# Performance work log

Measured on AMD Instinct MI355X. Metric: run time of the kernel, lower is better.

Reference implementation:

```python
import jax, jax.numpy as jnp
import numpy as np


def setup_inputs() -> dict:
    key = jax.random.key(0)
    k1, k2 = jax.random.split(key)
    bs, dim = 8192, 768
    nl_vec = jax.random.normal(k1, (bs, dim), dtype=jnp.float32)
    code_vec = jax.random.normal(k2, (bs, dim), dtype=jnp.float32)
    return {"nl_vec": nl_vec, "code_vec": code_vec}


def reference(nl_vec, code_vec):
    # scores[i, j] = <nl_vec[i], code_vec[j]>  (GEMM form of the broadcast mult-sum)
    scores = jnp.einsum("id,jd->ij", nl_vec, code_vec)  # [bs, bs]
    bs = scores.shape[0]
    # CrossEntropyLoss with labels = arange(bs): mean over rows of (logsumexp - diag)
    lse = jax.nn.logsumexp(scores, axis=-1)             # [bs]
    diag = jnp.einsum("id,id->i", nl_vec, code_vec)     # scores[i, i]
    loss = jnp.mean(lse - diag)
    return (loss, code_vec, nl_vec)
```

## Files before the change

### kernel.cpp

```cpp
#include <hip/hip_runtime.h>

#define BS     8192
#define DIM    768
#define NPART  32
#define BM     256
#define BN     256
#define BK     64
#define NKT    (DIM / BK)
#define L1B    128
#define L1R    (BS / L1B)

typedef __bf16 bfrag_t __attribute__((ext_vector_type(8)));
typedef float  facc_t  __attribute__((ext_vector_type(4)));

typedef const __attribute__((address_space(1))) void gv_t;
typedef __attribute__((address_space(3))) void lv_t;

__device__ __forceinline__ void gll16(const void* g, void* l) {
  __builtin_amdgcn_global_load_lds((gv_t*)g, (lv_t*)l, 16, 0, 0);
}

__device__ __forceinline__ unsigned short f2bf(float f) {
  union { float f; unsigned u; } v; v.f = f;
  unsigned u = v.u;
  return (unsigned short)((u + 0x7FFFu + ((u >> 16) & 1u)) >> 16);
}

__global__ void prep_kernel(const float* __restrict__ nl, const float* __restrict__ cd,
                            float* __restrict__ cd_copy, float* __restrict__ nl_copy,
                            unsigned short* __restrict__ nlb, unsigned short* __restrict__ cdb,
                            float* __restrict__ dg) {
  const int lane = threadIdx.x & 63;
  const int wave = threadIdx.x >> 6;
  const int row  = blockIdx.x * 4 + wave;
  const size_t rbase = (size_t)row * DIM;
  const float4* ar = reinterpret_cast<const float4*>(nl + rbase);
  const float4* br = reinterpret_cast<const float4*>(cd + rbase);
  float4* wa = reinterpret_cast<float4*>(nl_copy + rbase);
  float4* wb = reinterpret_cast<float4*>(cd_copy + rbase);
  ushort4* ba = reinterpret_cast<ushort4*>(nlb + rbase);
  ushort4* bb = reinterpret_cast<ushort4*>(cdb + rbase);

  float s = 0.f;
#pragma unroll
  for (int i = 0; i < 3; ++i) {
    int idx = lane + 64 * i;
    float4 x = ar[idx];
    float4 y = br[idx];
    wa[idx] = x;
    wb[idx] = y;
    ushort4 xb, yb;
    xb.x = f2bf(x.x); xb.y = f2bf(x.y); xb.z = f2bf(x.z); xb.w = f2bf(x.w);
    yb.x = f2bf(y.x); yb.y = f2bf(y.y); yb.z = f2bf(y.z); yb.w = f2bf(y.w);
    ba[idx] = xb;
    bb[idx] = yb;
    s += x.x * y.x + x.y * y.y + x.z * y.z + x.w * y.w;
  }
#pragma unroll
  for (int off = 32; off; off >>= 1) s += __shfl_xor(s, off, 64);
  if (lane == 0) dg[row] = s;
}

__global__ __launch_bounds__(512, 2) void gemm_lse_kernel(
    const unsigned short* __restrict__ Abf,
    const unsigned short* __restrict__ Bbf,
    float* __restrict__ pm, float* __restrict__ pl) {
  __shared__ __align__(16) unsigned short As[2 * BM * BK];
  __shared__ __align__(16) unsigned short Bs[2 * BN * BK];

  const int tid  = threadIdx.x;
  const int lane = tid & 63;
  const int wave = tid >> 6;
  const int wm   = wave >> 2;
  const int wn   = wave & 3;
  const int l15  = lane & 15;
  const int l4   = lane >> 4;
  const int swz  = l15 & 7;
  const int cb   = blockIdx.x;
  const int rb   = blockIdx.y;

  const int k8x0 = ((0 * 4 + l4) ^ swz) * 8;
  const int k8x1 = ((1 * 4 + l4) ^ swz) * 8;

  size_t aoff[4], boff[4];
  int ldso[4];
#pragma unroll
  for (int p = 0; p < 4; ++p) {
    int u   = p * 512 + tid;
    int row = u >> 3;
    int c8  = (u & 7) ^ (row & 7);
    aoff[p] = (size_t)(rb * BM + row) * DIM + c8 * 8;
    boff[p] = (size_t)(cb * BN + row) * DIM + c8 * 8;
    ldso[p] = u * 8;
  }

#define STG_A(kt, h) do { \
    gll16(Abf + aoff[2*(h)]   + (size_t)(kt) * BK, &As[(((kt) & 1) << 14) + ldso[2*(h)]]); \
    gll16(Abf + aoff[2*(h)+1] + (size_t)(kt) * BK, &As[(((kt) & 1) << 14) + ldso[2*(h)+1]]); \
  } while (0)
#define STG_B(kt, h) do { \
    gll16(Bbf + boff[2*(h)]   + (size_t)(kt) * BK, &Bs[(((kt) & 1) << 14) + ldso[2*(h)]]); \
    gll16(Bbf + boff[2*(h)+1] + (size_t)(kt) * BK, &Bs[(((kt) & 1) << 14) + ldso[2*(h)+1]]); \
  } while (0)

  bfrag_t af[2][2];
  bfrag_t bf[4][2];
  facc_t  acc[8][4];
#pragma unroll
  for (int mt = 0; mt < 8; ++mt)
#pragma unroll
    for (int nt = 0; nt < 4; ++nt) acc[mt][nt] = (facc_t){0.f, 0.f, 0.f, 0.f};

#define DS_A(b, q) do { \
    _Pragma("unroll") \
    for (int i_ = 0; i_ < 2; ++i_) { \
      const unsigned short* pA_ = &As[(b) * 16384 + (wm * 128 + (2*(q)+i_) * 16 + l15) * 64]; \
      af[i_][0] = *reinterpret_cast<const bfrag_t*>(pA_ + k8x0); \
      af[i_][1] = *reinterpret_cast<const bfrag_t*>(pA_ + k8x1); \
    } } while (0)
#define DS_B(b) do { \
    _Pragma("unroll") \
    for (int n_ = 0; n_ < 4; ++n_) { \
      const unsigned short* pB_ = &Bs[(b) * 16384 + (wn * 64 + n_ * 16 + l15) * 64]; \
      bf[n_][0] = *reinterpret_cast<const bfrag_t*>(pB_ + k8x0); \
      bf[n_][1] = *reinterpret_cast<const bfrag_t*>(pB_ + k8x1); \
    } } while (0)
#define MFMA_Q(q) do { \
    _Pragma("unroll") \
    for (int i_ = 0; i_ < 2; ++i_) \
      _Pragma("unroll") \
      for (int n_ = 0; n_ < 4; ++n_) { \
        acc[2*(q)+i_][n_] = __builtin_amdgcn_mfma_f32_16x16x32_bf16(af[i_][0], bf[n_][0], acc[2*(q)+i_][n_], 0, 0, 0); \
        acc[2*(q)+i_][n_] = __builtin_amdgcn_mfma_f32_16x16x32_bf16(af[i_][1], bf[n_][1], acc[2*(q)+i_][n_], 0, 0, 0); \
      } } while (0)

#define PH_TOP() do { __builtin_amdgcn_s_barrier(); \
    asm volatile("s_waitcnt lgkmcnt(0)" ::: "memory"); \
    __builtin_amdgcn_sched_barrier(0); \
    __builtin_amdgcn_s_setprio(1); } while (0)
#define PH_BOT() do { __builtin_amdgcn_s_setprio(0); \
    __builtin_amdgcn_sched_barrier(0); \
    __builtin_amdgcn_s_barrier(); } while (0)
#define PH_BOT_VM(n) do { __builtin_amdgcn_s_setprio(0); \
    __builtin_amdgcn_sched_barrier(0); \
    asm volatile("s_waitcnt vmcnt(" #n ")" ::: "memory"); \
    __builtin_amdgcn_sched_barrier(0); \
    __builtin_amdgcn_s_barrier(); } while (0)

  STG_B(0, 0); STG_B(0, 1); STG_A(0, 0); STG_A(0, 1); STG_B(1, 0); STG_B(1, 1);
  asm volatile("s_waitcnt vmcnt(4)" ::: "memory");
  __builtin_amdgcn_sched_barrier(0);
  __builtin_amdgcn_s_barrier();

  for (int t = 0; t < 5; ++t) {
    const int k0 = 2 * t;
    DS_B(0); DS_A(0, 0); STG_A(k0 + 1, 0); STG_A(k0 + 1, 1);
    PH_TOP(); MFMA_Q(0); PH_BOT();
    DS_A(0, 1); STG_B(k0 + 2, 0);
    PH_TOP(); MFMA_Q(1); PH_BOT();
    DS_A(0, 2); STG_B(k0 + 2, 1);
    PH_TOP(); MFMA_Q(2); PH_BOT();
    DS_A(0, 3);
    PH_TOP(); MFMA_Q(3); PH_BOT_VM(4);
    DS_B(1); DS_A(1, 0); STG_A(k0 + 2, 0);
    PH_TOP(); MFMA_Q(0); PH_BOT();
    DS_A(1, 1); STG_A(k0 + 2, 1);
    PH_TOP(); MFMA_Q(1); PH_BOT();
    DS_A(1, 2); STG_B(k0 + 3, 0);
    PH_TOP(); MFMA_Q(2); PH_BOT();
    DS_A(1, 3); STG_B(k0 + 3, 1);
    PH_TOP(); MFMA_Q(3); PH_BOT_VM(4);
  }

  DS_B(0); DS_A(0, 0); STG_A(11, 0); STG_A(11, 1);
  PH_TOP(); MFMA_Q(0); PH_BOT();
  DS_A(0, 1);
  PH_TOP(); MFMA_Q(1); PH_BOT();
  DS_A(0, 2);
  PH_TOP(); MFMA_Q(2); PH_BOT();
  DS_A(0, 3);
  PH_TOP(); MFMA_Q(3); PH_BOT_VM(0);
  DS_B(1); DS_A(1, 0);
  PH_TOP(); MFMA_Q(0); PH_BOT();
  DS_A(1, 1);
  PH_TOP(); MFMA_Q(1); PH_BOT();
  DS_A(1, 2);
  PH_TOP(); MFMA_Q(2); PH_BOT();
  DS_A(1, 3);
  PH_TOP(); MFMA_Q(3); PH_BOT();

  float* cm = reinterpret_cast<float*>(As);
  float* cl = reinterpret_cast<float*>(Bs);
#pragma unroll
  for (int mt = 0; mt < 8; ++mt)
#pragma unroll
    for (int r = 0; r < 4; ++r) {
      float v0 = acc[mt][0][r], v1 = acc[mt][1][r], v2 = acc[mt][2][r], v3 = acc[mt][3][r];
      float m = fmaxf(fmaxf(v0, v1), fmaxf(v2, v3));
      float l = __expf(v0 - m) + __expf(v1 - m) + __expf(v2 - m) + __expf(v3 - m);
#pragma unroll
      for (int mask = 1; mask < 16; mask <<= 1) {
        float om = __shfl_xor(m, mask, 64);
        float ol = __shfl_xor(l, mask, 64);
        float mn = fmaxf(m, om);
        l = l * __expf(m - mn) + ol * __expf(om - mn);
        m = mn;
      }
      if (l15 == 0) {
        int rl = wm * 128 + mt * 16 + l4 * 4 + r;
        cm[wn * BM + rl] = m;
        cl[wn * BM + rl] = l;
      }
    }
  __syncthreads();
  if (tid < BM) {
    float m0 = cm[tid],          l0 = cl[tid];
    float m1 = cm[BM + tid],     l1 = cl[BM + tid];
    float m2 = cm[2 * BM + tid], l2 = cl[2 * BM + tid];
    float m3 = cm[3 * BM + tid], l3 = cl[3 * BM + tid];
    float mn = fmaxf(fmaxf(m0, m1), fmaxf(m2, m3));
    float ll = l0 * __expf(m0 - mn) + l1 * __expf(m1 - mn) +
               l2 * __expf(m2 - mn) + l3 * __expf(m3 - mn);
    size_t g = (size_t)(rb * BM + tid) * NPART + cb;
    pm[g] = mn;
    pl[g] = ll;
  }

#undef STG_A
#undef STG_B
#undef DS_A
#undef DS_B
#undef MFMA_Q
#undef PH_TOP
#undef PH_BOT
#undef PH_BOT_VM
}

__global__ void loss_stage1_kernel(const float* __restrict__ pm, const float* __restrict__ pl,
                                   const float* __restrict__ dg, float* __restrict__ partial) {
  const int tid = threadIdx.x;
  const int r   = blockIdx.x * L1R + tid;

  const float4* pmr = reinterpret_cast<const float4*>(pm + (size_t)r * NPART);
  const float4* plr = reinterpret_cast<const float4*>(pl + (size_t)r * NPART);

  float m = -1e30f, l = 0.f;
#pragma unroll
  for (int q = 0; q < NPART / 4; ++q) {
    float4 mv = pmr[q];
    float4 lv = plr[q];
#pragma unroll
    for (int k = 0; k < 4; ++k) {
      float m2 = (&mv.x)[k], l2 = (&lv.x)[k];
      float mn = fmaxf(m, m2);
      l = l * __expf(m - mn) + l2 * __expf(m2 - mn);
      m = mn;
    }
  }
  float local = m + __logf(l) - dg[r];

#pragma unroll
  for (int off = 32; off; off >>= 1) local += __shfl_xor(local, off, 64);
  if (tid == 0) partial[blockIdx.x] = local;
}

__global__ void loss_stage2_kernel(const float* __restrict__ partial, float* __restrict__ out) {
  const int tid = threadIdx.x;
  float v = partial[tid];
#pragma unroll
  for (int off = 32; off; off >>= 1) v += __shfl_xor(v, off, 64);
  __shared__ float red[2];
  if ((tid & 63) == 0) red[tid >> 6] = v;
  __syncthreads();
  if (tid == 0) out[0] = (red[0] + red[1]) / (float)BS;
}

extern "C" void kernel_launch(void* const* d_in, const int* in_sizes, int n_in,
                              void* d_out, int out_size, void* d_ws, size_t ws_size,
                              hipStream_t stream) {
  const float* nl = (const float*)d_in[0];
  const float* cd = (const float*)d_in[1];
  float* out = (float*)d_out;

  const size_t NEL = (size_t)BS * DIM;

  unsigned short* nlb = (unsigned short*)d_ws;
  unsigned short* cdb = nlb + NEL;
  float* pm = (float*)(cdb + NEL);
  float* pl = pm + (size_t)BS * NPART;
  float* dg = pl + (size_t)BS * NPART;
  float* partial = dg + BS;

  prep_kernel<<<BS / 4, 256, 0, stream>>>(nl, cd, out + 1, out + 1 + NEL, nlb, cdb, dg);
  gemm_lse_kernel<<<dim3(NPART, BS / BM), 512, 0, stream>>>(nlb, cdb, pm, pl);
  loss_stage1_kernel<<<L1B, 64, 0, stream>>>(pm, pl, dg, partial);
  loss_stage2_kernel<<<1, 128, 0, stream>>>(partial, out);
}
```

Before: 251.5 us.

## Rework GEMM main loop to triple-buffered BK=32 pipeline with inline-asm LDS reads

```diff
diff --git a/kernel.cpp b/kernel.cpp
--- a/kernel.cpp
+++ b/kernel.cpp
@@ -5,13 +5,14 @@
 #define NPART  32
 #define BM     256
 #define BN     256
-#define BK     64
+#define BK     32
 #define NKT    (DIM / BK)
 #define L1B    128
 #define L1R    (BS / L1B)
 
 typedef __bf16 bfrag_t __attribute__((ext_vector_type(8)));
 typedef float  facc_t  __attribute__((ext_vector_type(4)));
+typedef float  f4raw   __attribute__((ext_vector_type(4)));
 
 typedef const __attribute__((address_space(1))) void gv_t;
 typedef __attribute__((address_space(3))) void lv_t;
@@ -65,8 +66,7 @@
     const unsigned short* __restrict__ Abf,
     const unsigned short* __restrict__ Bbf,
     float* __restrict__ pm, float* __restrict__ pl) {
-  __shared__ __align__(16) unsigned short As[2 * BM * BK];
-  __shared__ __align__(16) unsigned short Bs[2 * BN * BK];
+  __shared__ __align__(16) unsigned short LDSU[49152];
 
   const int tid  = threadIdx.x;
   const int lane = tid & 63;
@@ -75,122 +75,104 @@
   const int wn   = wave & 3;
   const int l15  = lane & 15;
   const int l4   = lane >> 4;
-  const int swz  = l15 & 7;
-  const int cb   = blockIdx.x;
-  const int rb   = blockIdx.y;
-
-  const int k8x0 = ((0 * 4 + l4) ^ swz) * 8;
-  const int k8x1 = ((1 * 4 + l4) ^ swz) * 8;
-
-  size_t aoff[4], boff[4];
-  int ldso[4];
-#pragma unroll
-  for (int p = 0; p < 4; ++p) {
-    int u   = p * 512 + tid;
-    int row = u >> 3;
-    int c8  = (u & 7) ^ (row & 7);
-    aoff[p] = (size_t)(rb * BM + row) * DIM + c8 * 8;
-    boff[p] = (size_t)(cb * BN + row) * DIM + c8 * 8;
-    ldso[p] = u * 8;
-  }
-
-#define STG_A(kt, h) do { \
-    gll16(Abf + aoff[2*(h)]   + (size_t)(kt) * BK, &As[(((kt) & 1) << 14) + ldso[2*(h)]]); \
-    gll16(Abf + aoff[2*(h)+1] + (size_t)(kt) * BK, &As[(((kt) & 1) << 14) + ldso[2*(h)+1]]); \
-  } while (0)
-#define STG_B(kt, h) do { \
-    gll16(Bbf + boff[2*(h)]   + (size_t)(kt) * BK, &Bs[(((kt) & 1) << 14) + ldso[2*(h)]]); \
-    gll16(Bbf + boff[2*(h)+1] + (size_t)(kt) * BK, &Bs[(((kt) & 1) << 14) + ldso[2*(h)+1]]); \
-  } while (0)
-
-  bfrag_t af[2][2];
-  bfrag_t bf[4][2];
-  facc_t  acc[8][4];
+
+  unsigned lin = blockIdx.y * 32 + blockIdx.x;
+  unsigned swz = (lin & 7) * 128 + (lin >> 3);
+  const int cb = swz & 31;
+  const int rb = swz >> 5;
+
+  const int a0_ = tid >> 3, s0_ = tid & 7, l0_ = s0_ ^ (a0_ & 7);
+  const int grow = 2 * a0_ + ((l0_ >> 2) & 1);
+  const int gc8  = l0_ & 3;
+  const unsigned short* srcA0 = Abf + (size_t)(rb * BM + grow) * DIM + gc8 * 8;
+  const unsigned short* srcB0 = Bbf + (size_t)(cb * BN + grow) * DIM + gc8 * 8;
+  char* dstA0 = (char*)LDSU + tid * 16;
+  char* dstB0 = (char*)LDSU + 49152 + tid * 16;
+
+#define STGA(k) do{ gll16(srcA0 + (size_t)(k) * 32,                    dstA0 + ((k) % 3) * 16384); \
+                    gll16(srcA0 + (size_t)128 * DIM + (size_t)(k) * 32, dstA0 + ((k) % 3) * 16384 + 8192);}while(0)
+#define STGB(k) do{ gll16(srcB0 + (size_t)(k) * 32,                    dstB0 + ((k) % 3) * 16384); \
+                    gll16(srcB0 + (size_t)128 * DIM + (size_t)(k) * 32, dstB0 + ((k) % 3) * 16384 + 8192);}while(0)
+
+  const unsigned lds32 = (unsigned)(uintptr_t)(void*)&LDSU[0];
+  const unsigned physA = ((unsigned)(((l15 & 1) << 2) | l4)) ^ (unsigned)((l15 >> 1) & 7);
+  const unsigned abase = lds32 + (unsigned)(wm * 64 + (l15 >> 1)) * 128 + physA * 16;
+  const unsigned bbase = lds32 + 49152u + (unsigned)(wn * 32 + (l15 >> 1)) * 128 + physA * 16;
+
+  f4raw afL[4], afH[4], bfE[4], bfO[4];
+  facc_t acc[8][4];
 #pragma unroll
   for (int mt = 0; mt < 8; ++mt)
 #pragma unroll
     for (int nt = 0; nt < 4; ++nt) acc[mt][nt] = (facc_t){0.f, 0.f, 0.f, 0.f};
 
-#define DS_A(b, q) do { \
+#define DSR(dst, addr, off) \
+  asm volatile("ds_read_b128 %0, %1 offset:%2" : "=v"(dst) : "v"(addr), "n"(off))
+#define RD4(ARR, base, off) do{ \
+    DSR(ARR[0], base, (off) + 0 * 1024); DSR(ARR[1], base, (off) + 1 * 1024); \
+    DSR(ARR[2], base, (off) + 2 * 1024); DSR(ARR[3], base, (off) + 3 * 1024); }while(0)
+
+#define MFMA_PH(AF, BF, half) do{ \
     _Pragma("unroll") \
-    for (int i_ = 0; i_ < 2; ++i_) { \
-      const unsigned short* pA_ = &As[(b) * 16384 + (wm * 128 + (2*(q)+i_) * 16 + l15) * 64]; \
-      af[i_][0] = *reinterpret_cast<const bfrag_t*>(pA_ + k8x0); \
-      af[i_][1] = *reinterpret_cast<const bfrag_t*>(pA_ + k8x1); \
-    } } while (0)
-#define DS_B(b) do { \
-    _Pragma("unroll") \
-    for (int n_ = 0; n_ < 4; ++n_) { \
-      const unsigned short* pB_ = &Bs[(b) * 16384 + (wn * 64 + n_ * 16 + l15) * 64]; \
-      bf[n_][0] = *reinterpret_cast<const bfrag_t*>(pB_ + k8x0); \
-      bf[n_][1] = *reinterpret_cast<const bfrag_t*>(pB_ + k8x1); \
-    } } while (0)
-#define MFMA_Q(q) do { \
-    _Pragma("unroll") \
-    for (int i_ = 0; i_ < 2; ++i_) \
+    for (int m_ = 0; m_ < 4; ++m_) \
       _Pragma("unroll") \
-      for (int n_ = 0; n_ < 4; ++n_) { \
-        acc[2*(q)+i_][n_] = __builtin_amdgcn_mfma_f32_16x16x32_bf16(af[i_][0], bf[n_][0], acc[2*(q)+i_][n_], 0, 0, 0); \
-        acc[2*(q)+i_][n_] = __builtin_amdgcn_mfma_f32_16x16x32_bf16(af[i_][1], bf[n_][1], acc[2*(q)+i_][n_], 0, 0, 0); \
-      } } while (0)
-
-#define PH_TOP() do { __builtin_amdgcn_s_barrier(); \
-    asm volatile("s_waitcnt lgkmcnt(0)" ::: "memory"); \
-    __builtin_amdgcn_sched_barrier(0); \
-    __builtin_amdgcn_s_setprio(1); } while (0)
-#define PH_BOT() do { __builtin_amdgcn_s_setprio(0); \
-    __builtin_amdgcn_sched_barrier(0); \
-    __builtin_amdgcn_s_barrier(); } while (0)
-#define PH_BOT_VM(n) do { __builtin_amdgcn_s_setprio(0); \
-    __builtin_amdgcn_sched_barrier(0); \
-    asm volatile("s_waitcnt vmcnt(" #n ")" ::: "memory"); \
-    __builtin_amdgcn_sched_barrier(0); \
-    __builtin_amdgcn_s_barrier(); } while (0)
-
-  STG_B(0, 0); STG_B(0, 1); STG_A(0, 0); STG_A(0, 1); STG_B(1, 0); STG_B(1, 1);
-  asm volatile("s_waitcnt vmcnt(4)" ::: "memory");
+      for (int n_ = 0; n_ < 4; ++n_) \
+        acc[(half) * 4 + m_][n_] = __builtin_amdgcn_mfma_f32_16x16x32_bf16( \
+            __builtin_bit_cast(bfrag_t, AF[m_]), __builtin_bit_cast(bfrag_t, BF[n_]), \
+            acc[(half) * 4 + m_][n_], 0, 0, 0); \
+  }while(0)
+
+#define TOPN(n) do{ __builtin_amdgcn_sched_barrier(0); __builtin_amdgcn_s_barrier(); \
+    asm volatile("s_waitcnt lgkmcnt(" #n ")"); __builtin_amdgcn_sched_barrier(0); \
+    __builtin_amdgcn_s_setprio(1);}while(0)
+#define BOT() do{ __builtin_amdgcn_s_setprio(0); __builtin_amdgcn_sched_barrier(0); \
+    __builtin_amdgcn_s_barrier();}while(0)
+#define BOTVM(n) do{ __builtin_amdgcn_s_setprio(0); __builtin_amdgcn_sched_barrier(0); \
+    asm volatile("s_waitcnt vmcnt(" #n ")"); __builtin_amdgcn_sched_barrier(0); \
+    __builtin_amdgcn_s_barrier();}while(0)
+
+#define KT(k, BFC, BFN, VMN) do{ \
+     \
+    RD4(afH, abase, ((k) % 3) * 16384 + 4096); \
+    if ((k) <= 21) STGA((k) + 2); \
+    TOPN(4); \
+    MFMA_PH(afL, BFC, 0); \
+    BOTVM(VMN);                                    \
+     \
+    RD4(BFN, bbase, (((k) + 1) % 3) * 16384); \
+    RD4(afL, abase, (((k) + 1) % 3) * 16384); \
+    if ((k) <= 21) STGB((k) + 2); \
+    TOPN(8); \
+    MFMA_PH(afH, BFC, 1); \
+    BOT(); \
+  }while(0)
+
+  STGA(0); STGB(0); STGA(1); STGB(1);
+  __builtin_amdgcn_sched_barrier(0);
+  asm volatile("s_waitcnt vmcnt(4)");
   __builtin_amdgcn_sched_barrier(0);
   __builtin_amdgcn_s_barrier();
-
-  for (int t = 0; t < 5; ++t) {
-    const int k0 = 2 * t;
-    DS_B(0); DS_A(0, 0); STG_A(k0 + 1, 0); STG_A(k0 + 1, 1);
-    PH_TOP(); MFMA_Q(0); PH_BOT();
-    DS_A(0, 1); STG_B(k0 + 2, 0);
-    PH_TOP(); MFMA_Q(1); PH_BOT();
-    DS_A(0, 2); STG_B(k0 + 2, 1);
-    PH_TOP(); MFMA_Q(2); PH_BOT();
-    DS_A(0, 3);
-    PH_TOP(); MFMA_Q(3); PH_BOT_VM(4);
-    DS_B(1); DS_A(1, 0); STG_A(k0 + 2, 0);
-    PH_TOP(); MFMA_Q(0); PH_BOT();
-    DS_A(1, 1); STG_A(k0 + 2, 1);
-    PH_TOP(); MFMA_Q(1); PH_BOT();
-    DS_A(1, 2); STG_B(k0 + 3, 0);
-    PH_TOP(); MFMA_Q(2); PH_BOT();
-    DS_A(1, 3); STG_B(k0 + 3, 1);
-    PH_TOP(); MFMA_Q(3); PH_BOT_VM(4);
-  }
-
-  DS_B(0); DS_A(0, 0); STG_A(11, 0); STG_A(11, 1);
-  PH_TOP(); MFMA_Q(0); PH_BOT();
-  DS_A(0, 1);
-  PH_TOP(); MFMA_Q(1); PH_BOT();
-  DS_A(0, 2);
-  PH_TOP(); MFMA_Q(2); PH_BOT();
-  DS_A(0, 3);
-  PH_TOP(); MFMA_Q(3); PH_BOT_VM(0);
-  DS_B(1); DS_A(1, 0);
-  PH_TOP(); MFMA_Q(0); PH_BOT();
-  DS_A(1, 1);
-  PH_TOP(); MFMA_Q(1); PH_BOT();
-  DS_A(1, 2);
-  PH_TOP(); MFMA_Q(2); PH_BOT();
-  DS_A(1, 3);
-  PH_TOP(); MFMA_Q(3); PH_BOT();
-
-  float* cm = reinterpret_cast<float*>(As);
-  float* cl = reinterpret_cast<float*>(Bs);
+  RD4(bfE, bbase, 0);
+  RD4(afL, abase, 0);
+
+  KT(0,  bfE, bfO, 2); KT(1,  bfO, bfE, 2); KT(2,  bfE, bfO, 2); KT(3,  bfO, bfE, 2);
+  KT(4,  bfE, bfO, 2); KT(5,  bfO, bfE, 2); KT(6,  bfE, bfO, 2); KT(7,  bfO, bfE, 2);
+  KT(8,  bfE, bfO, 2); KT(9,  bfO, bfE, 2); KT(10, bfE, bfO, 2); KT(11, bfO, bfE, 2);
+  KT(12, bfE, bfO, 2); KT(13, bfO, bfE, 2); KT(14, bfE, bfO, 2); KT(15, bfO, bfE, 2);
+  KT(16, bfE, bfO, 2); KT(17, bfO, bfE, 2); KT(18, bfE, bfO, 2); KT(19, bfO, bfE, 2);
+  KT(20, bfE, bfO, 2); KT(21, bfO, bfE, 2); KT(22, bfE, bfO, 0);
+
+  RD4(afH, abase, 2 * 16384 + 4096);
+  TOPN(4);
+  MFMA_PH(afL, bfO, 0);
+  BOT();
+  TOPN(0);
+  MFMA_PH(afH, bfO, 1);
+  BOT();
+
+  float* cm = reinterpret_cast<float*>(LDSU);
+  float* cl = reinterpret_cast<float*>(LDSU + 2048);
+  __syncthreads();
 #pragma unroll
   for (int mt = 0; mt < 8; ++mt)
 #pragma unroll
@@ -226,14 +208,15 @@
     pl[g] = ll;
   }
 
-#undef STG_A
-#undef STG_B
-#undef DS_A
-#undef DS_B
-#undef MFMA_Q
-#undef PH_TOP
-#undef PH_BOT
-#undef PH_BOT_VM
+#undef STGA
+#undef STGB
+#undef DSR
+#undef RD4
+#undef MFMA_PH
+#undef TOPN
+#undef BOT
+#undef BOTVM
+#undef KT
 }
 
 __global__ void loss_stage1_kernel(const float* __restrict__ pm, const float* __restrict__ pl,
@@ -292,7 +275,7 @@
   float* partial = dg + BS;
 
   prep_kernel<<<BS / 4, 256, 0, stream>>>(nl, cd, out + 1, out + 1 + NEL, nlb, cdb, dg);
-  gemm_lse_kernel<<<dim3(NPART, BS / BM), 512, 0, stream>>>(nlb, cdb, pm, pl);
+  gemm_lse_kernel<<<dim3(32, 32), 512, 0, stream>>>(nlb, cdb, pm, pl);
   loss_stage1_kernel<<<L1B, 64, 0, stream>>>(pm, pl, dg, partial);
   loss_stage2_kernel<<<1, 128, 0, stream>>>(partial, out);
 }
```

Result: faster. 229.7 us (-8.7%).
